# Optimization experiments

Measured on AMD Instinct MI355X. Metric: run time of the kernel, lower is better.

The kernel has to match this reference:

```python
import jax, jax.numpy as jnp
import numpy as np

NP_, NA_, E_ = 100000, 100000, 3200000
DIN, HID, OUT = 128, 8, 7


def setup_inputs():
    ks = jax.random.split(jax.random.key(0), 32)
    n = lambda i, s: jax.random.normal(ks[i], s, dtype=jnp.float32) * 0.1
    z = lambda s: jnp.zeros(s, jnp.float32)
    return {
        "x_paper": jax.random.normal(ks[0], (NP_, DIN), dtype=jnp.float32),
        "x_author": jax.random.normal(ks[1], (NA_, DIN), dtype=jnp.float32),
        "ei_pp": jax.random.randint(ks[2], (2, E_), 0, NP_),
        "ei_pa": jnp.stack([jax.random.randint(ks[3], (E_,), 0, NP_),
                            jax.random.randint(ks[4], (E_,), 0, NA_)]),
        "ei_ap": jnp.stack([jax.random.randint(ks[5], (E_,), 0, NA_),
                            jax.random.randint(ks[6], (E_,), 0, NP_)]),
        "w1_paper": n(7, (DIN, HID)), "b1_paper": z((HID,)),
        "w1_author": n(8, (DIN, HID)), "b1_author": z((HID,)),
        "asrc1_pp": n(9, (2, 4)), "adst1_pp": n(10, (2, 4)),
        "asrc1_pa": n(11, (2, 4)), "adst1_pa": n(12, (2, 4)),
        "asrc1_ap": n(13, (2, 4)), "adst1_ap": n(14, (2, 4)),
        "kw1": n(15, (HID, HID)), "kb1": z((HID,)), "q1": n(16, (HID,)),
        "w2_paper": n(17, (HID, OUT)), "b2_paper": z((OUT,)),
        "w2_author": n(18, (HID, OUT)), "b2_author": z((OUT,)),
        "asrc2_pp": n(19, (1, OUT)), "adst2_pp": n(20, (1, OUT)),
        "asrc2_pa": n(21, (1, OUT)), "adst2_pa": n(22, (1, OUT)),
        "asrc2_ap": n(23, (1, OUT)), "adst2_ap": n(24, (1, OUT)),
        "kw2": n(25, (OUT, OUT)), "kb2": z((OUT,)), "q2": n(26, (OUT,)),
    }


def _seg_softmax(a, seg, num):
    # segment softmax over incoming edges per destination node (PyG softmax util)
    m = jax.ops.segment_max(a, seg, num_segments=num)
    ex = jnp.exp(a - m[seg])
    s = jax.ops.segment_sum(ex, seg, num_segments=num)
    return ex / (s[seg] + 1e-16)


def _han_edge(x_src, x_dst, src, dst, a_src_p, a_dst_p, n_dst):
    # x_src/x_dst: [N, H, D]; a_*_p: [H, D]
    a = (x_src * a_src_p).sum(-1)[src] + (x_dst * a_dst_p).sum(-1)[dst]  # [E, H]
    a = _seg_softmax(jax.nn.leaky_relu(a, 0.2), dst, n_dst)
    msg = (x_src[src] * a[:, :, None]).reshape(src.shape[0], -1)         # [E, H*D]
    return jax.nn.relu(jax.ops.segment_sum(msg, dst, num_segments=n_dst))


def _group(outs, q, kw, kb):
    # semantic attention over edge-type outputs (PyG HANConv `group`)
    o = jnp.stack(outs)                                                  # [T, N, F]
    attn = jax.nn.softmax((q * jnp.tanh(o @ kw + kb).mean(1)).sum(-1))   # [T]
    return jnp.einsum('t,tnf->nf', attn, o)


def _han_layer(xd, eis, w, b, a_s, a_d, q, kw, kb, H, F):
    D = F // H
    xp = {nt: (xd[nt] @ w[nt] + b[nt]).reshape(-1, H, D) for nt in xd}
    outs = {nt: [] for nt in xd}
    for (st, dt), ei in eis.items():
        outs[dt].append(_han_edge(xp[st], xp[dt], ei[0], ei[1],
                                  a_s[(st, dt)], a_d[(st, dt)], xd[dt].shape[0]))
    return {nt: _group(outs[nt], q, kw, kb) for nt in xd}


def reference(x_paper, x_author, ei_pp, ei_pa, ei_ap,
              w1_paper, b1_paper, w1_author, b1_author,
              asrc1_pp, adst1_pp, asrc1_pa, adst1_pa, asrc1_ap, adst1_ap, kw1, kb1, q1,
              w2_paper, b2_paper, w2_author, b2_author,
              asrc2_pp, adst2_pp, asrc2_pa, adst2_pa, asrc2_ap, adst2_ap, kw2, kb2, q2):
    eis = {("paper", "paper"): ei_pp, ("paper", "author"): ei_pa, ("author", "paper"): ei_ap}
    xd = {"paper": x_paper, "author": x_author}
    xd = _han_layer(xd, eis,
                    {"paper": w1_paper, "author": w1_author},
                    {"paper": b1_paper, "author": b1_author},
                    {("paper", "paper"): asrc1_pp, ("paper", "author"): asrc1_pa, ("author", "paper"): asrc1_ap},
                    {("paper", "paper"): adst1_pp, ("paper", "author"): adst1_pa, ("author", "paper"): adst1_ap},
                    q1, kw1, kb1, 2, HID)
    xd = {k: jax.nn.relu(v) for k, v in xd.items()}   # HetGraphNet inter-layer ReLU
    xd = _han_layer(xd, eis,
                    {"paper": w2_paper, "author": w2_author},
                    {"paper": b2_paper, "author": b2_author},
                    {("paper", "paper"): asrc2_pp, ("paper", "author"): asrc2_pa, ("author", "paper"): asrc2_ap},
                    {("paper", "paper"): adst2_pp, ("paper", "author"): adst2_pa, ("author", "paper"): adst2_ap},
                    q2, kw2, kb2, 1, OUT)
    # node-level task, multiclass classification, log_probs return type
    return jax.nn.log_softmax(xd["paper"], axis=-1)
```

## Files before the change

### kernel.cpp

```cpp
#include <hip/hip_runtime.h>

constexpr int DIN = 128, HIDF = 8;
constexpr int LOGD = 8, DPB = 1 << LOGD;
constexpr int BE = 8192;
constexpr int NBCAP = 512;
constexpr int SCAP = 16384;

__device__ inline unsigned bfpack(float lo, float hi) {
  unsigned a = __float_as_uint(lo), b = __float_as_uint(hi);
  unsigned ra = (a + 0x7fffu + ((a >> 16) & 1u)) >> 16;
  unsigned rb = (b + 0x7fffu + ((b >> 16) & 1u)) >> 16;
  return ra | (rb << 16);
}
__device__ inline float bflo(unsigned u) { return __uint_as_float(u << 16); }
__device__ inline float bfhi(unsigned u) { return __uint_as_float(u & 0xffff0000u); }

__global__ __launch_bounds__(256) void k_proj1(
    const float* __restrict__ x, const float* __restrict__ w,
    const float* __restrict__ b, float* __restrict__ xp, int N)
{
  __shared__ float ws_[DIN * HIDF];
  __shared__ float xs[32 * 132];
  int t = threadIdx.x;
  ((float4*)ws_)[t] = ((const float4*)w)[t];
  int base = blockIdx.x * 32;
#pragma unroll
  for (int i = 0; i < 4; i++) {
    int f4 = t + i * 256;
    int nl = f4 >> 5;
    if (base + nl < N) {
      float4 v = ((const float4*)(x + (size_t)base * DIN))[f4];
      int col = (f4 & 31) << 2;
      *((float4*)&xs[nl * 132 + col]) = v;
    }
  }
  __syncthreads();
  int nl = t >> 3, j = t & 7;
  int n0 = base + nl;
  if (n0 >= N) return;
  float acc = b[j];
  const float* xr = &xs[nl * 132];
#pragma unroll 8
  for (int k = 0; k < DIN; k++) acc = fmaf(xr[k], ws_[k * HIDF + j], acc);
  xp[(size_t)n0 * HIDF + j] = acc;
}

__global__ __launch_bounds__(256) void k_pack1(
    const float* __restrict__ xp, int N,
    const float* __restrict__ ps0, float* __restrict__ rec0,
    const float* __restrict__ ps1, float* __restrict__ rec1,
    const float* __restrict__ pd0, float* __restrict__ od0,
    const float* __restrict__ pd1, float* __restrict__ od1)
{
  int n = blockIdx.x * blockDim.x + threadIdx.x;
  if (n >= N) return;
  float4 a4 = ((const float4*)xp)[(size_t)n * 2];
  float4 b4 = ((const float4*)xp)[(size_t)n * 2 + 1];
  float xv[8] = {a4.x, a4.y, a4.z, a4.w, b4.x, b4.y, b4.z, b4.w};
  uint4 pk;
  pk.x = bfpack(xv[0], xv[1]); pk.y = bfpack(xv[2], xv[3]);
  pk.z = bfpack(xv[4], xv[5]); pk.w = bfpack(xv[6], xv[7]);
#define DOT2(p, s0, s1)                                               \
  float s0 = 0.f, s1 = 0.f;                                           \
  for (int d = 0; d < 4; d++) { s0 += xv[d] * p[d]; s1 += xv[4 + d] * p[4 + d]; }
  if (rec0) {
    DOT2(ps0, s0, s1)
    ((uint4*)rec0)[(size_t)n * 2] = pk;
    ((float4*)rec0)[(size_t)n * 2 + 1] = make_float4(s0, s1, 0.f, 0.f);
  }
  if (rec1) {
    DOT2(ps1, s0, s1)
    ((uint4*)rec1)[(size_t)n * 2] = pk;
    ((float4*)rec1)[(size_t)n * 2 + 1] = make_float4(s0, s1, 0.f, 0.f);
  }
  if (pd0) { DOT2(pd0, s0, s1) ((float2*)od0)[n] = make_float2(s0, s1); }
  if (pd1) { DOT2(pd1, s0, s1) ((float2*)od1)[n] = make_float2(s0, s1); }
#undef DOT2
}

__global__ __launch_bounds__(512) void k_bcount(
    const int* __restrict__ d0, const int* __restrict__ d1, const int* __restrict__ d2,
    int E, int nblocks, int* __restrict__ PB1)
{
  int ty = blockIdx.y;
  const int* dst = ty == 0 ? d0 : (ty == 1 ? d1 : d2);
  __shared__ int hist[NBCAP];
  int t = threadIdx.x;
  hist[t] = 0;
  __syncthreads();
  int blk = blockIdx.x;
  int e0 = blk * BE, e1 = min(E, e0 + BE);
  int qbase = e0 >> 2, nq = (e1 - e0) >> 2;
#pragma unroll
  for (int i = 0; i < 4; i++) {
    int q = i * 512 + t;
    if (q < nq) {
      int4 v = ((const int4*)dst)[qbase + q];
      atomicAdd(&hist[v.x >> LOGD], 1);
      atomicAdd(&hist[v.y >> LOGD], 1);
      atomicAdd(&hist[v.z >> LOGD], 1);
      atomicAdd(&hist[v.w >> LOGD], 1);
    }
  }
  __syncthreads();
  PB1[((size_t)(ty * NBCAP) + t) * nblocks + blk] = hist[t];
}

__global__ __launch_bounds__(512) void k_bscan(
    int* __restrict__ PB1, int* __restrict__ TOTS,
    int nblocks, int NBmax, int nb0, int nb1, int nb2)
{
  int ty = blockIdx.y;
  int NBt = ty == 0 ? nb0 : (ty == 1 ? nb1 : nb2);
  int bk = blockIdx.x;
  if (bk >= NBt) return;
  int* p = PB1 + ((size_t)(ty * NBCAP) + bk) * nblocks;
  int t = threadIdx.x;
  int v = (t < nblocks) ? p[t] : 0;
  int lane = t & 63, wv = t >> 6;
  int x = v;
#pragma unroll
  for (int o = 1; o < 64; o <<= 1) { int u = __shfl_up(x, o, 64); if (lane >= o) x += u; }
  __shared__ int ws[8];
  if (lane == 63) ws[wv] = x;
  __syncthreads();
  if (t == 0) { int s = 0; for (int k = 0; k < 8; k++) { int tmp = ws[k]; ws[k] = s; s += tmp; } }
  __syncthreads();
  int excl = x - v + ws[wv];
  if (t < nblocks) p[t] = excl;
  if (t == nblocks - 1) TOTS[ty * NBmax + bk] = excl + v;
}

__global__ __launch_bounds__(512) void k_bstart(
    const int* __restrict__ TOTS, int* __restrict__ BSTART,
    int NBmax, int nb0, int nb1, int nb2)
{
  int ty = blockIdx.x;
  int NBt = ty == 0 ? nb0 : (ty == 1 ? nb1 : nb2);
  int t = threadIdx.x;
  int v = (t < NBt) ? TOTS[ty * NBmax + t] : 0;
  int lane = t & 63, wv = t >> 6;
  int x = v;
#pragma unroll
  for (int o = 1; o < 64; o <<= 1) { int u = __shfl_up(x, o, 64); if (lane >= o) x += u; }
  __shared__ int ws[8];
  if (lane == 63) ws[wv] = x;
  __syncthreads();
  if (t == 0) { int s = 0; for (int k = 0; k < 8; k++) { int tmp = ws[k]; ws[k] = s; s += tmp; } }
  __syncthreads();
  int excl = x - v + ws[wv];
  int* bs = BSTART + (size_t)ty * (NBmax + 1);
  if (t < NBt) bs[t] = excl;
  if (t == NBt - 1) bs[NBt] = excl + v;
}

__global__ __launch_bounds__(512) void k_bplace(
    const int* __restrict__ e0p, const int* __restrict__ e1p, const int* __restrict__ e2p,
    int E, int nblocks, int NBmax, int nb0, int nb1, int nb2,
    const int* __restrict__ PB1, const int* __restrict__ BSTART,
    int* __restrict__ PART)
{
  int ty = blockIdx.y;
  const int* src = ty == 0 ? e0p : (ty == 1 ? e1p : e2p);
  const int* dst = src + E;
  int NBt = ty == 0 ? nb0 : (ty == 1 ? nb1 : nb2);
  int* part = PART + (size_t)ty * E;
  __shared__ int hist[NBCAP];
  __shared__ int lscan[NBCAP + 1];
  __shared__ int bpref[NBCAP];
  __shared__ int bst[NBCAP];
  __shared__ int stage[BE];
  __shared__ int ws[8];
  int t = threadIdx.x;
  hist[t] = 0;
  __syncthreads();
  int blk = blockIdx.x;
  int e0 = blk * BE, e1 = min(E, e0 + BE);
  int cnt = e1 - e0;
  int qbase = e0 >> 2, nq = cnt >> 2;
  int dreg[16], sreg[16];
  unsigned short lr[16];
#pragma unroll
  for (int i = 0; i < 4; i++) {
    int q = i * 512 + t;
    if (q < nq) {
      int4 dq = ((const int4*)dst)[qbase + q];
      int4 sq = ((const int4*)src)[qbase + q];
      dreg[i * 4 + 0] = dq.x; dreg[i * 4 + 1] = dq.y;
      dreg[i * 4 + 2] = dq.z; dreg[i * 4 + 3] = dq.w;
      sreg[i * 4 + 0] = sq.x; sreg[i * 4 + 1] = sq.y;
      sreg[i * 4 + 2] = sq.z; sreg[i * 4 + 3] = sq.w;
#pragma unroll
      for (int k = 0; k < 4; k++)
        lr[i * 4 + k] = (unsigned short)atomicAdd(&hist[dreg[i * 4 + k] >> LOGD], 1);
    } else {
#pragma unroll
      for (int k = 0; k < 4; k++) dreg[i * 4 + k] = -1;
    }
  }
  __syncthreads();
  {
    int v = hist[t];
    int lane = t & 63, wv = t >> 6;
    int x = v;
#pragma unroll
    for (int o = 1; o < 64; o <<= 1) { int u = __shfl_up(x, o, 64); if (lane >= o) x += u; }
    if (lane == 63) ws[wv] = x;
    __syncthreads();
    if (t == 0) { int s = 0; for (int k = 0; k < 8; k++) { int tmp = ws[k]; ws[k] = s; s += tmp; } }
    __syncthreads();
    int excl = x - v + ws[wv];
    lscan[t] = excl;
    if (t == NBCAP - 1) lscan[NBCAP] = excl + v;
  }
  if (t < NBt) {
    bpref[t] = PB1[((size_t)(ty * NBCAP) + t) * nblocks + blk];
    bst[t] = BSTART[(size_t)ty * (NBmax + 1) + t];
  }
  __syncthreads();
#pragma unroll
  for (int i = 0; i < 16; i++) {
    int d = dreg[i];
    if (d >= 0) {
      int bk = d >> LOGD;
      stage[lscan[bk] + lr[i]] = (sreg[i] << LOGD) | (d & (DPB - 1));
    }
  }
  __syncthreads();
  for (int j = t; j < cnt; j += 512) {
    int lo = 0, hi = NBt - 1;
    while (lo < hi) { int mid = (lo + hi + 1) >> 1; if (lscan[mid] <= j) lo = mid; else hi = mid - 1; }
    part[bst[lo] + bpref[lo] + (j - lscan[lo])] = stage[j];
  }
}

__global__ __launch_bounds__(512) void k_sort(
    int* __restrict__ PART, const int* __restrict__ BSTART, int NBmax, int E,
    int nb0, int nb1, int nb2, int n0, int n1, int n2,
    int nmx1, int* __restrict__ OFFs)
{
  int ty = blockIdx.y;
  int NBt = ty == 0 ? nb0 : (ty == 1 ? nb1 : nb2);
  int Nt  = ty == 0 ? n0 : (ty == 1 ? n1 : n2);
  int bk = blockIdx.x;
  if (bk >= NBt) return;
  int* part = PART + (size_t)ty * E;
  const int* bs = BSTART + (size_t)ty * (NBmax + 1);
  int s0 = bs[bk], s1 = bs[bk + 1];
  int cnt = s1 - s0;
  __shared__ int hist[DPB];
  __shared__ int binoff[DPB];
  __shared__ int sorted[SCAP];
  __shared__ int ws[4];
  int t = threadIdx.x;
  if (t < DPB) hist[t] = 0;
  __syncthreads();
  int myv[32];
  unsigned short myr[32];
#pragma unroll
  for (int it = 0; it < 32; it++) {
    int j = s0 + it * 512 + t;
    if (j < s1) {
      int v = part[j];
      myv[it] = v;
      myr[it] = (unsigned short)atomicAdd(&hist[v & (DPB - 1)], 1);
    } else myv[it] = -1;
  }
  __syncthreads();
  {
    int v = (t < DPB) ? hist[t] : 0;
    int lane = t & 63, wv = t >> 6;
    int x = v;
#pragma unroll
    for (int o = 1; o < 64; o <<= 1) { int u = __shfl_up(x, o, 64); if (lane >= o) x += u; }
    if (t < DPB && lane == 63) ws[wv] = x;
    __syncthreads();
    if (t == 0) { int s = 0; for (int k = 0; k < 4; k++) { int tmp = ws[k]; ws[k] = s; s += tmp; } }
    __syncthreads();
    if (t < DPB) binoff[t] = x - v + ws[wv];
  }
  __syncthreads();
  int d0 = bk << LOGD;
  if (t < DPB && d0 + t < Nt) OFFs[(size_t)ty * nmx1 + d0 + t] = s0 + binoff[t];
  if (bk == NBt - 1 && t == 0) OFFs[(size_t)ty * nmx1 + Nt] = s1;
#pragma unroll
  for (int it = 0; it < 32; it++) {
    int v = myv[it];
    if (v >= 0) sorted[binoff[v & (DPB - 1)] + myr[it]] = v >> LOGD;
  }
  __syncthreads();
  for (int j = t; j < cnt; j += 512) part[s0 + j] = sorted[j];
}

__global__ __launch_bounds__(512) void k_gather1(
    const int* __restrict__ PART, const int* __restrict__ OFFs, int nmx1, int E, int gG,
    const float* __restrict__ r0, const float* __restrict__ ad0, float* __restrict__ o0, int n0,
    const float* __restrict__ r1, const float* __restrict__ ad1, float* __restrict__ o1, int n1,
    const float* __restrict__ r2, const float* __restrict__ ad2, float* __restrict__ o2, int n2)
{
  int bid = blockIdx.x;
  int rr = bid & 7, m = bid >> 3;
  int ty, xb;
  if (rr < 3)      { ty = 0; xb = m * 3 + rr; }
  else if (rr < 6) { ty = 1; xb = m * 3 + (rr - 3); }
  else             { ty = 2; xb = m * 2 + (rr - 6); }
  if (xb >= gG) return;
  const float* rec = ty == 0 ? r0 : (ty == 1 ? r1 : r2);
  const float* ad_ = ty == 0 ? ad0 : (ty == 1 ? ad1 : ad2);
  float* out = ty == 0 ? o0 : (ty == 1 ? o1 : o2);
  int Nt = ty == 0 ? n0 : (ty == 1 ? n1 : n2);
  int g = xb * 512 + threadIdx.x;
  int d = g >> 4, l = g & 15;
  if (d >= Nt) return;
  const int* off = OFFs + (size_t)ty * nmx1;
  const int* part = PART + (size_t)ty * E;
  int i0 = off[d], i1 = off[d + 1];
  float2 adv = ((const float2*)ad_)[d];
  float s0 = 0.f, s1 = 0.f;
  float acc[8] = {0.f, 0.f, 0.f, 0.f, 0.f, 0.f, 0.f, 0.f};
  for (int i = i0 + l; i < i1; i += 16) {
    int s = part[i];
    uint4 q = ((const uint4*)rec)[(size_t)s * 2];
    float4 ax = ((const float4*)rec)[(size_t)s * 2 + 1];
    float a0 = ax.x + adv.x; a0 = a0 > 0.f ? a0 : 0.2f * a0;
    float a1 = ax.y + adv.y; a1 = a1 > 0.f ? a1 : 0.2f * a1;
    float e0 = __expf(a0), e1 = __expf(a1);
    s0 += e0; s1 += e1;
    acc[0] += e0 * bflo(q.x); acc[1] += e0 * bfhi(q.x);
    acc[2] += e0 * bflo(q.y); acc[3] += e0 * bfhi(q.y);
    acc[4] += e1 * bflo(q.z); acc[5] += e1 * bfhi(q.z);
    acc[6] += e1 * bflo(q.w); acc[7] += e1 * bfhi(q.w);
  }
#pragma unroll
  for (int mm = 1; mm < 16; mm <<= 1) {
    s0 += __shfl_xor(s0, mm, 16);
    s1 += __shfl_xor(s1, mm, 16);
#pragma unroll
    for (int k = 0; k < 8; k++) acc[k] += __shfl_xor(acc[k], mm, 16);
  }
  if (l) return;
  float r0i = 1.f / (s0 + 1e-16f), r1i = 1.f / (s1 + 1e-16f);
  float4 q0 = make_float4(fmaxf(acc[0] * r0i, 0.f), fmaxf(acc[1] * r0i, 0.f),
                          fmaxf(acc[2] * r0i, 0.f), fmaxf(acc[3] * r0i, 0.f));
  float4 q1 = make_float4(fmaxf(acc[4] * r1i, 0.f), fmaxf(acc[5] * r1i, 0.f),
                          fmaxf(acc[6] * r1i, 0.f), fmaxf(acc[7] * r1i, 0.f));
  ((float4*)out)[(size_t)d * 2] = q0;
  ((float4*)out)[(size_t)d * 2 + 1] = q1;
}

__global__ __launch_bounds__(512) void k_gather2(
    const int* __restrict__ PART, const int* __restrict__ OFFs, int nmx1, int E,
    int ti0, int ti1,
    const float* __restrict__ r0, const float* __restrict__ ad0, float* __restrict__ o0,
    const float* __restrict__ r1, const float* __restrict__ ad1, float* __restrict__ o1, int N)
{
  int zz = blockIdx.y;
  int ty = zz == 0 ? ti0 : ti1;
  const float* rec = zz == 0 ? r0 : r1;
  const float* ad_ = zz == 0 ? ad0 : ad1;
  float* out = zz == 0 ? o0 : o1;
  int g = blockIdx.x * 512 + threadIdx.x;
  int d = g >> 4, l = g & 15;
  if (d >= N) return;
  const int* off = OFFs + (size_t)ty * nmx1;
  const int* part = PART + (size_t)ty * E;
  int i0 = off[d], i1 = off[d + 1];
  float adv = ad_[d];
  float ssum = 0.f;
  float acc[7] = {0.f, 0.f, 0.f, 0.f, 0.f, 0.f, 0.f};
  for (int i = i0 + l; i < i1; i += 16) {
    int s = part[i];
    uint4 q = ((const uint4*)rec)[s];
    float a = bfhi(q.w) + adv; a = a > 0.f ? a : 0.2f * a;
    float ex = __expf(a);
    ssum += ex;
    acc[0] += ex * bflo(q.x); acc[1] += ex * bfhi(q.x);
    acc[2] += ex * bflo(q.y); acc[3] += ex * bfhi(q.y);
    acc[4] += ex * bflo(q.z); acc[5] += ex * bfhi(q.z);
    acc[6] += ex * bflo(q.w);
  }
#pragma unroll
  for (int mm = 1; mm < 16; mm <<= 1) {
    ssum += __shfl_xor(ssum, mm, 16);
#pragma unroll
    for (int k = 0; k < 7; k++) acc[k] += __shfl_xor(acc[k], mm, 16);
  }
  if (l) return;
  float r = 1.f / (ssum + 1e-16f);
  float4 q0 = make_float4(fmaxf(acc[0] * r, 0.f), fmaxf(acc[1] * r, 0.f),
                          fmaxf(acc[2] * r, 0.f), fmaxf(acc[3] * r, 0.f));
  float4 q1 = make_float4(fmaxf(acc[4] * r, 0.f), fmaxf(acc[5] * r, 0.f),
                          fmaxf(acc[6] * r, 0.f), 0.f);
  ((float4*)out)[(size_t)d * 2] = q0;
  ((float4*)out)[(size_t)d * 2 + 1] = q1;
}

__global__ __launch_bounds__(256) void k_red(
    const float* __restrict__ hA, const float* __restrict__ hB, int N, int F,
    const float* __restrict__ kw, const float* __restrict__ kb,
    float* __restrict__ redA, float* __restrict__ redB)
{
  const float* h = blockIdx.y ? hB : hA;
  float* red = blockIdx.y ? redB : redA;
  __shared__ float kws[64], kbs[8];
  __shared__ float sm[256 * 8];
  int t = threadIdx.x;
  if (t < F * F) kws[t] = kw[t];
  if (t < F) kbs[t] = kb[t];
  __syncthreads();
  float acc[8] = {0, 0, 0, 0, 0, 0, 0, 0};
  for (int n = blockIdx.x * 256 + t; n < N; n += gridDim.x * 256) {
    const float* row = h + (size_t)n * 8;
    float xv[8];
    for (int k = 0; k < F; k++) xv[k] = row[k];
    for (int f = 0; f < F; f++) {
      float s = kbs[f];
      for (int k = 0; k < F; k++) s += xv[k] * kws[k * F + f];
      acc[f] += tanhf(s);
    }
  }
  for (int f = 0; f < 8; f++) sm[t * 8 + f] = (f < F) ? acc[f] : 0.f;
  __syncthreads();
  for (int s2 = 128; s2 > 0; s2 >>= 1) {
    if (t < s2)
      for (int f = 0; f < 8; f++) sm[t * 8 + f] += sm[(t + s2) * 8 + f];
    __syncthreads();
  }
  if (t < F) atomicAdd(&red[t], sm[t]);
}

__global__ void k_attn(const float* __restrict__ red, const float* __restrict__ q,
                       int T, int F, float invN, float* __restrict__ attn)
{
  if (threadIdx.x != 0 || blockIdx.x != 0) return;
  float v[4]; float m = -1e30f;
  for (int t2 = 0; t2 < T; t2++) {
    float s = 0.f;
    for (int f = 0; f < F; f++) s += q[f] * red[t2 * F + f];
    s *= invN;
    v[t2] = s; m = fmaxf(m, s);
  }
  float sum = 0.f;
  for (int t2 = 0; t2 < T; t2++) { v[t2] = __expf(v[t2] - m); sum += v[t2]; }
  for (int t2 = 0; t2 < T; t2++) attn[t2] = v[t2] / sum;
}

__global__ __launch_bounds__(256) void k_proj2(
    const float* __restrict__ h0, const float* __restrict__ h1,
    const float* __restrict__ attn, int N,
    const float* __restrict__ w, const float* __restrict__ b,
    float* __restrict__ rec2, const float* __restrict__ psrc,
    const float* __restrict__ pd0, float* __restrict__ od0,
    const float* __restrict__ pd1, float* __restrict__ od1)
{
  int n = blockIdx.x * blockDim.x + threadIdx.x;
  if (n >= N) return;
  float a0 = 1.f, a1 = 0.f;
  if (attn) { a0 = attn[0]; a1 = attn[1]; }
  float4 u0 = ((const float4*)h0)[(size_t)n * 2];
  float4 u1 = ((const float4*)h0)[(size_t)n * 2 + 1];
  float xv[8] = {u0.x, u0.y, u0.z, u0.w, u1.x, u1.y, u1.z, u1.w};
  if (h1) {
    float4 v0 = ((const float4*)h1)[(size_t)n * 2];
    float4 v1 = ((const float4*)h1)[(size_t)n * 2 + 1];
    float yv[8] = {v0.x, v0.y, v0.z, v0.w, v1.x, v1.y, v1.z, v1.w};
    for (int j = 0; j < 8; j++) xv[j] = a0 * xv[j] + a1 * yv[j];
  }
  for (int j = 0; j < 8; j++) xv[j] = fmaxf(xv[j], 0.f);
  float y[7];
  for (int j = 0; j < 7; j++) y[j] = b[j];
  for (int k = 0; k < 8; k++) {
    float xk = xv[k];
    for (int j = 0; j < 7; j++) y[j] += xk * w[k * 7 + j];
  }
  float ssrc = 0.f;
  for (int j = 0; j < 7; j++) ssrc += y[j] * psrc[j];
  uint4 pk;
  pk.x = bfpack(y[0], y[1]); pk.y = bfpack(y[2], y[3]);
  pk.z = bfpack(y[4], y[5]); pk.w = bfpack(y[6], ssrc);
  ((uint4*)rec2)[n] = pk;
#define DOD(p, o)                                       \
  if (p) {                                              \
    float s = 0.f;                                      \
    for (int j = 0; j < 7; j++) s += y[j] * p[j];       \
    o[n] = s;                                           \
  }
  DOD(pd0, od0) DOD(pd1, od1)
#undef DOD
}

__global__ __launch_bounds__(256) void k_final(
    const float* __restrict__ h0, const float* __restrict__ h1,
    const float* __restrict__ attn, float* __restrict__ out, int N)
{
  int n = blockIdx.x * blockDim.x + threadIdx.x;
  if (n >= N) return;
  float a0 = attn[0], a1 = attn[1];
  const float* r0 = h0 + (size_t)n * 8;
  const float* r1 = h1 + (size_t)n * 8;
  float v[7]; float m = -1e30f;
  for (int c = 0; c < 7; c++) { float t = a0 * r0[c] + a1 * r1[c]; v[c] = t; m = fmaxf(m, t); }
  float sum = 0.f;
  for (int c = 0; c < 7; c++) sum += __expf(v[c] - m);
  float lse = m + logf(sum);
  for (int c = 0; c < 7; c++) out[(size_t)n * 7 + c] = v[c] - lse;
}

extern "C" void kernel_launch(void* const* d_in, const int* in_sizes, int n_in,
                              void* d_out, int out_size, void* d_ws, size_t ws_size,
                              hipStream_t stream)
{
  const float* x_p  = (const float*)d_in[0];
  const float* x_a  = (const float*)d_in[1];
  const int*   eipp = (const int*)d_in[2];
  const int*   eipa = (const int*)d_in[3];
  const int*   eiap = (const int*)d_in[4];
  const float* w1p  = (const float*)d_in[5];
  const float* b1p  = (const float*)d_in[6];
  const float* w1a  = (const float*)d_in[7];
  const float* b1a  = (const float*)d_in[8];
  const float* as1pp = (const float*)d_in[9];
  const float* ad1pp = (const float*)d_in[10];
  const float* as1pa = (const float*)d_in[11];
  const float* ad1pa = (const float*)d_in[12];
  const float* as1ap = (const float*)d_in[13];
  const float* ad1ap = (const float*)d_in[14];
  const float* kw1 = (const float*)d_in[15];
  const float* kb1 = (const float*)d_in[16];
  const float* q1  = (const float*)d_in[17];
  const float* w2p = (const float*)d_in[18];
  const float* b2p = (const float*)d_in[19];
  const float* w2a = (const float*)d_in[20];
  const float* b2a = (const float*)d_in[21];
  const float* as2pp = (const float*)d_in[22];
  const float* ad2pp = (const float*)d_in[23];
  const float* as2ap = (const float*)d_in[26];
  const float* ad2ap = (const float*)d_in[27];
  const float* kw2 = (const float*)d_in[28];
  const float* kb2 = (const float*)d_in[29];
  const float* q2  = (const float*)d_in[30];

  const int NP = in_sizes[0] / DIN;
  const int NA = in_sizes[1] / DIN;
  const int E  = in_sizes[2] / 2;
  (void)n_in; (void)out_size; (void)ws_size;

  const int nblocks = (E + BE - 1) / BE;
  const int NBp = (NP + DPB - 1) >> LOGD;
  const int NBa = (NA + DPB - 1) >> LOGD;
  const int NBmax = NBp > NBa ? NBp : NBa;
  const int nmx  = NP > NA ? NP : NA;
  const int nmx1 = nmx + 1;

  float* w = (float*)d_ws;
  size_t off_ = 0;
  auto A = [&](size_t n) { float* p = w + off_; off_ += (n + 15) & ~(size_t)15; return p; };
  float* XP_P1 = A((size_t)NP * 8);
  float* XP_A1 = A((size_t)NA * 8);
  float* RECPP = A((size_t)NP * 8);
  float* RECPA = A((size_t)NP * 8);
  float* RECAP = A((size_t)NA * 8);
  float* AD_PP = A((size_t)NP * 2);
  float* AD_PA = A((size_t)NA * 2);
  float* AD_AP = A((size_t)NP * 2);
  float* A2DPP = A((size_t)NP);
  float* A2DAP = A((size_t)NP);
  float* O_PP  = A((size_t)NP * 8);
  float* O_PA  = A((size_t)NA * 8);
  float* O_AP  = A((size_t)NP * 8);
  float* ATT1  = A(2);
  float* ATT2  = A(2);
  float* RED1  = A(16);
  float* RED2  = A(16);
  int* PART   = (int*)A((size_t)3 * E);
  int* PB1    = (int*)A((size_t)3 * NBCAP * nblocks);
  int* TOTS   = (int*)A((size_t)3 * NBmax);
  int* BSTART = (int*)A((size_t)3 * (NBmax + 1));
  int* OFFs   = (int*)A((size_t)3 * nmx1);

  float* REC2P = RECPP;
  float* REC2A = RECAP;
  float* O2PP  = O_PP;
  float* O2AP  = O_AP;

  hipMemsetAsync(RED1, 0, 32 * sizeof(float), stream);

  dim3 B(256);
  int nbP = (NP + 255) / 256, nbA = (NA + 255) / 256;
  int gG = (nmx * 16 + 511) / 512;
  int g1blocks = 8 * ((gG + 1) / 2);

  k_proj1<<<(NP + 31) / 32, B, 0, stream>>>(x_p, w1p, b1p, XP_P1, NP);
  k_proj1<<<(NA + 31) / 32, B, 0, stream>>>(x_a, w1a, b1a, XP_A1, NA);
  k_pack1<<<nbP, B, 0, stream>>>(XP_P1, NP,
      as1pp, RECPP, as1pa, RECPA, ad1pp, AD_PP, ad1ap, AD_AP);
  k_pack1<<<nbA, B, 0, stream>>>(XP_A1, NA,
      as1ap, RECAP, nullptr, nullptr, ad1pa, AD_PA, nullptr, nullptr);

  k_bcount<<<dim3(nblocks, 3), dim3(512), 0, stream>>>(
      eipp + E, eipa + E, eiap + E, E, nblocks, PB1);
  k_bscan<<<dim3(NBmax, 3), dim3(512), 0, stream>>>(
      PB1, TOTS, nblocks, NBmax, NBp, NBa, NBp);
  k_bstart<<<3, dim3(512), 0, stream>>>(TOTS, BSTART, NBmax, NBp, NBa, NBp);
  k_bplace<<<dim3(nblocks, 3), dim3(512), 0, stream>>>(
      eipp, eipa, eiap, E, nblocks, NBmax, NBp, NBa, NBp, PB1, BSTART, PART);
  k_sort<<<dim3(NBmax, 3), dim3(512), 0, stream>>>(
      PART, BSTART, NBmax, E, NBp, NBa, NBp, NP, NA, NP, nmx1, OFFs);

  k_gather1<<<dim3(g1blocks), dim3(512), 0, stream>>>(
      PART, OFFs, nmx1, E, gG,
      RECPP, AD_PP, O_PP, NP,
      RECPA, AD_PA, O_PA, NA,
      RECAP, AD_AP, O_AP, NP);

  k_red<<<dim3(256, 2), B, 0, stream>>>(O_PP, O_AP, NP, 8, kw1, kb1, RED1, RED1 + 8);
  k_attn<<<1, 1, 0, stream>>>(RED1, q1, 2, 8, 1.0f / NP, ATT1);

  k_proj2<<<nbP, B, 0, stream>>>(O_PP, O_AP, ATT1, NP, w2p, b2p,
      REC2P, as2pp, ad2pp, A2DPP, ad2ap, A2DAP);
  k_proj2<<<nbA, B, 0, stream>>>(O_PA, nullptr, nullptr, NA, w2a, b2a,
      REC2A, as2ap, nullptr, nullptr, nullptr, nullptr);

  k_gather2<<<dim3((NP * 16 + 511) / 512, 2), dim3(512), 0, stream>>>(
      PART, OFFs, nmx1, E, 0, 2,
      REC2P, A2DPP, O2PP,
      REC2A, A2DAP, O2AP, NP);

  k_red<<<dim3(256, 2), B, 0, stream>>>(O2PP, O2AP, NP, 7, kw2, kb2, RED2, RED2 + 7);
  k_attn<<<1, 1, 0, stream>>>(RED2, q2, 2, 7, 1.0f / NP, ATT2);
  k_final<<<nbP, B, 0, stream>>>(O2PP, O2AP, ATT2, (float*)d_out, NP);
}
```

Measured before the change: 316.5 us.

## Use 8 lanes per node with 4-way unrolled gathers and bucket lookup table

The gather kernels now assign 8 lanes per destination node instead of 16 and unroll each lane's edge loop four ways, using masked duplicate loads for the tail, so more independent loads are in flight per lane and the shuffle reduction is shorter. The bucket-placement kernel replaces the per-element binary search over bucket prefixes with a shared-memory table mapping each staged slot to its bucket, plus a precombined base offset. The added shared table costs extra LDS and occupancy. Masked tail iterations waste some loads and exp work on nodes with low degree.

Result: slower. 339.7 us (+7.3%).

```diff
diff --git a/kernel.cpp b/kernel.cpp
--- a/kernel.cpp
+++ b/kernel.cpp
@@ -167,9 +167,9 @@
   int* part = PART + (size_t)ty * E;
   __shared__ int hist[NBCAP];
   __shared__ int lscan[NBCAP + 1];
-  __shared__ int bpref[NBCAP];
-  __shared__ int bst[NBCAP];
+  __shared__ int base[NBCAP];
   __shared__ int stage[BE];
+  __shared__ short bkt[BE];
   __shared__ int ws[8];
   int t = threadIdx.x;
   hist[t] = 0;
@@ -213,25 +213,29 @@
     lscan[t] = excl;
     if (t == NBCAP - 1) lscan[NBCAP] = excl + v;
   }
-  if (t < NBt) {
-    bpref[t] = PB1[((size_t)(ty * NBCAP) + t) * nblocks + blk];
-    bst[t] = BSTART[(size_t)ty * (NBmax + 1) + t];
-  }
-  __syncthreads();
+  if (t < NBt)
+    base[t] = BSTART[(size_t)ty * (NBmax + 1) + t]
+            + PB1[((size_t)(ty * NBCAP) + t) * nblocks + blk];
+  __syncthreads();
+  {
+    int b = t;
+    if (b < NBt) {
+      int j0 = lscan[b], j1 = lscan[b + 1];
+      base[b] -= j0;
+      for (int j = j0; j < j1; j++) bkt[j] = (short)b;
+    }
+  }
 #pragma unroll
   for (int i = 0; i < 16; i++) {
     int d = dreg[i];
     if (d >= 0) {
-      int bk = d >> LOGD;
-      stage[lscan[bk] + lr[i]] = (sreg[i] << LOGD) | (d & (DPB - 1));
+      int bk2 = d >> LOGD;
+      stage[lscan[bk2] + lr[i]] = (sreg[i] << LOGD) | (d & (DPB - 1));
     }
   }
   __syncthreads();
-  for (int j = t; j < cnt; j += 512) {
-    int lo = 0, hi = NBt - 1;
-    while (lo < hi) { int mid = (lo + hi + 1) >> 1; if (lscan[mid] <= j) lo = mid; else hi = mid - 1; }
-    part[bst[lo] + bpref[lo] + (j - lscan[lo])] = stage[j];
-  }
+  for (int j = t; j < cnt; j += 512)
+    part[base[bkt[j]] + j] = stage[j];
 }
 
 __global__ __launch_bounds__(512) void k_sort(
@@ -310,7 +314,7 @@
   float* out = ty == 0 ? o0 : (ty == 1 ? o1 : o2);
   int Nt = ty == 0 ? n0 : (ty == 1 ? n1 : n2);
   int g = xb * 512 + threadIdx.x;
-  int d = g >> 4, l = g & 15;
+  int d = g >> 3, l = g & 7;
   if (d >= Nt) return;
   const int* off = OFFs + (size_t)ty * nmx1;
   const int* part = PART + (size_t)ty * E;
@@ -318,25 +322,40 @@
   float2 adv = ((const float2*)ad_)[d];
   float s0 = 0.f, s1 = 0.f;
   float acc[8] = {0.f, 0.f, 0.f, 0.f, 0.f, 0.f, 0.f, 0.f};
-  for (int i = i0 + l; i < i1; i += 16) {
-    int s = part[i];
-    uint4 q = ((const uint4*)rec)[(size_t)s * 2];
-    float4 ax = ((const float4*)rec)[(size_t)s * 2 + 1];
-    float a0 = ax.x + adv.x; a0 = a0 > 0.f ? a0 : 0.2f * a0;
-    float a1 = ax.y + adv.y; a1 = a1 > 0.f ? a1 : 0.2f * a1;
-    float e0 = __expf(a0), e1 = __expf(a1);
-    s0 += e0; s1 += e1;
-    acc[0] += e0 * bflo(q.x); acc[1] += e0 * bfhi(q.x);
-    acc[2] += e0 * bflo(q.y); acc[3] += e0 * bfhi(q.y);
-    acc[4] += e1 * bflo(q.z); acc[5] += e1 * bfhi(q.z);
-    acc[6] += e1 * bflo(q.w); acc[7] += e1 * bfhi(q.w);
-  }
-#pragma unroll
-  for (int mm = 1; mm < 16; mm <<= 1) {
-    s0 += __shfl_xor(s0, mm, 16);
-    s1 += __shfl_xor(s1, mm, 16);
-#pragma unroll
-    for (int k = 0; k < 8; k++) acc[k] += __shfl_xor(acc[k], mm, 16);
+
+#define EDGE1(sidx, msk)                                                 \
+  {                                                                      \
+    uint4 q = ((const uint4*)rec)[(size_t)(sidx) * 2];                   \
+    float4 ax = ((const float4*)rec)[(size_t)(sidx) * 2 + 1];            \
+    float a0 = ax.x + adv.x; a0 = a0 > 0.f ? a0 : 0.2f * a0;             \
+    float a1 = ax.y + adv.y; a1 = a1 > 0.f ? a1 : 0.2f * a1;             \
+    float e0 = __expf(a0) * (msk), e1 = __expf(a1) * (msk);              \
+    s0 += e0; s1 += e1;                                                  \
+    acc[0] += e0 * bflo(q.x); acc[1] += e0 * bfhi(q.x);                  \
+    acc[2] += e0 * bflo(q.y); acc[3] += e0 * bfhi(q.y);                  \
+    acc[4] += e1 * bflo(q.z); acc[5] += e1 * bfhi(q.z);                  \
+    acc[6] += e1 * bflo(q.w); acc[7] += e1 * bfhi(q.w);                  \
+  }
+
+  for (int i = i0 + l; i < i1; i += 32) {
+    int ja = i, jb = i + 8, jc = i + 16, jd = i + 24;
+    int sa = part[ja];
+    int sb = jb < i1 ? part[jb] : sa;
+    int sc = jc < i1 ? part[jc] : sa;
+    int sd = jd < i1 ? part[jd] : sa;
+    float mb = jb < i1 ? 1.f : 0.f;
+    float mc = jc < i1 ? 1.f : 0.f;
+    float md = jd < i1 ? 1.f : 0.f;
+    EDGE1(sa, 1.f) EDGE1(sb, mb) EDGE1(sc, mc) EDGE1(sd, md)
+  }
+#undef EDGE1
+
+#pragma unroll
+  for (int mm = 1; mm < 8; mm <<= 1) {
+    s0 += __shfl_xor(s0, mm, 8);
+    s1 += __shfl_xor(s1, mm, 8);
+#pragma unroll
+    for (int k = 0; k < 8; k++) acc[k] += __shfl_xor(acc[k], mm, 8);
   }
   if (l) return;
   float r0i = 1.f / (s0 + 1e-16f), r1i = 1.f / (s1 + 1e-16f);
@@ -360,7 +379,7 @@
   const float* ad_ = zz == 0 ? ad0 : ad1;
   float* out = zz == 0 ? o0 : o1;
   int g = blockIdx.x * 512 + threadIdx.x;
-  int d = g >> 4, l = g & 15;
+  int d = g >> 3, l = g & 7;
   if (d >= N) return;
   const int* off = OFFs + (size_t)ty * nmx1;
   const int* part = PART + (size_t)ty * E;
@@ -368,22 +387,37 @@
   float adv = ad_[d];
   float ssum = 0.f;
   float acc[7] = {0.f, 0.f, 0.f, 0.f, 0.f, 0.f, 0.f};
-  for (int i = i0 + l; i < i1; i += 16) {
-    int s = part[i];
-    uint4 q = ((const uint4*)rec)[s];
-    float a = bfhi(q.w) + adv; a = a > 0.f ? a : 0.2f * a;
-    float ex = __expf(a);
-    ssum += ex;
-    acc[0] += ex * bflo(q.x); acc[1] += ex * bfhi(q.x);
-    acc[2] += ex * bflo(q.y); acc[3] += ex * bfhi(q.y);
-    acc[4] += ex * bflo(q.z); acc[5] += ex * bfhi(q.z);
-    acc[6] += ex * bflo(q.w);
-  }
-#pragma unroll
-  for (int mm = 1; mm < 16; mm <<= 1) {
-    ssum += __shfl_xor(ssum, mm, 16);
-#pragma unroll
-    for (int k = 0; k < 7; k++) acc[k] += __shfl_xor(acc[k], mm, 16);
+
+#define EDGE2(sidx, msk)                                                 \
+  {                                                                      \
+    uint4 q = ((const uint4*)rec)[sidx];                                 \
+    float a = bfhi(q.w) + adv; a = a > 0.f ? a : 0.2f * a;               \
+    float ex = __expf(a) * (msk);                                        \
+    ssum += ex;                                                          \
+    acc[0] += ex * bflo(q.x); acc[1] += ex * bfhi(q.x);                  \
+    acc[2] += ex * bflo(q.y); acc[3] += ex * bfhi(q.y);                  \
+    acc[4] += ex * bflo(q.z); acc[5] += ex * bfhi(q.z);                  \
+    acc[6] += ex * bflo(q.w);                                            \
+  }
+
+  for (int i = i0 + l; i < i1; i += 32) {
+    int ja = i, jb = i + 8, jc = i + 16, jd = i + 24;
+    int sa = part[ja];
+    int sb = jb < i1 ? part[jb] : sa;
+    int sc = jc < i1 ? part[jc] : sa;
+    int sd = jd < i1 ? part[jd] : sa;
+    float mb = jb < i1 ? 1.f : 0.f;
+    float mc = jc < i1 ? 1.f : 0.f;
+    float md = jd < i1 ? 1.f : 0.f;
+    EDGE2(sa, 1.f) EDGE2(sb, mb) EDGE2(sc, mc) EDGE2(sd, md)
+  }
+#undef EDGE2
+
+#pragma unroll
+  for (int mm = 1; mm < 8; mm <<= 1) {
+    ssum += __shfl_xor(ssum, mm, 8);
+#pragma unroll
+    for (int k = 0; k < 7; k++) acc[k] += __shfl_xor(acc[k], mm, 8);
   }
   if (l) return;
   float r = 1.f / (ssum + 1e-16f);
@@ -587,7 +621,7 @@
 
   dim3 B(256);
   int nbP = (NP + 255) / 256, nbA = (NA + 255) / 256;
-  int gG = (nmx * 16 + 511) / 512;
+  int gG = (nmx * 8 + 511) / 512;
   int g1blocks = 8 * ((gG + 1) / 2);
 
   k_proj1<<<(NP + 31) / 32, B, 0, stream>>>(x_p, w1p, b1p, XP_P1, NP);
@@ -621,7 +655,7 @@
   k_proj2<<<nbA, B, 0, stream>>>(O_PA, nullptr, nullptr, NA, w2a, b2a,
       REC2A, as2ap, nullptr, nullptr, nullptr, nullptr);
 
-  k_gather2<<<dim3((NP * 16 + 511) / 512, 2), dim3(512), 0, stream>>>(
+  k_gather2<<<dim3((NP * 8 + 511) / 512, 2), dim3(512), 0, stream>>>(
       PART, OFFs, nmx1, E, 0, 2,
       REC2P, A2DPP, O2PP,
       REC2A, A2DAP, O2AP, NP);
```
